# Performance work log

Hardware: AMD Instinct MI355X
Metric: run time of the kernel (lower is better)

The kernel has to match this reference:

```python
import jax, jax.numpy as jnp
import numpy as np

B, N, K, H = 2, 2048, 48, 128
SCALE = 30.0
LN_EPS = 1e-5


def _gather_nodes(nodes, idx):
    # nodes: [B,N,H], idx: [B,N,K] -> [B,N,K,H]
    return nodes[jnp.arange(nodes.shape[0])[:, None, None], idx]


def _ln(x, g, b):
    m = jnp.mean(x, axis=-1, keepdims=True)
    v = jnp.mean(jnp.square(x - m), axis=-1, keepdims=True)
    return (x - m) * jax.lax.rsqrt(v + LN_EPS) * g + b


def _gelu(x):
    return jax.nn.gelu(x, approximate=False)  # torch.nn.GELU default (erf)


def setup_inputs() -> dict:
    key = jax.random.key(0)
    ks = jax.random.split(key, 24)
    d = {}
    d["h_V"] = jax.random.normal(ks[0], (B, N, H), jnp.float32)
    d["h_E"] = jax.random.normal(ks[1], (B, N, K, H), jnp.float32)
    d["E_idx"] = jax.random.randint(ks[2], (B, N, K), 0, N)
    d["mask_V"] = (jax.random.uniform(ks[3], (B, N)) > 0.1).astype(jnp.float32)
    d["mask_attend"] = (jax.random.uniform(ks[4], (B, N, K)) > 0.1).astype(jnp.float32)
    s = 0.05
    # message MLP (node update): W1 in = 3H
    d["W1_w"] = s * jax.random.normal(ks[5], (3 * H, H), jnp.float32)
    d["W1_b"] = jnp.zeros((H,), jnp.float32)
    d["W2_w"] = s * jax.random.normal(ks[6], (H, H), jnp.float32)
    d["W2_b"] = jnp.zeros((H,), jnp.float32)
    d["W3_w"] = s * jax.random.normal(ks[7], (H, H), jnp.float32)
    d["W3_b"] = jnp.zeros((H,), jnp.float32)
    # message MLP (edge update)
    d["W11_w"] = s * jax.random.normal(ks[8], (3 * H, H), jnp.float32)
    d["W11_b"] = jnp.zeros((H,), jnp.float32)
    d["W12_w"] = s * jax.random.normal(ks[9], (H, H), jnp.float32)
    d["W12_b"] = jnp.zeros((H,), jnp.float32)
    d["W13_w"] = s * jax.random.normal(ks[10], (H, H), jnp.float32)
    d["W13_b"] = jnp.zeros((H,), jnp.float32)
    # FFN
    d["Win_w"] = s * jax.random.normal(ks[11], (H, 4 * H), jnp.float32)
    d["Win_b"] = jnp.zeros((4 * H,), jnp.float32)
    d["Wout_w"] = s * jax.random.normal(ks[12], (4 * H, H), jnp.float32)
    d["Wout_b"] = jnp.zeros((H,), jnp.float32)
    # layernorms
    for i, nm in enumerate(["ln1", "ln2", "ln3"]):
        d[nm + "_g"] = jnp.ones((H,), jnp.float32)
        d[nm + "_b"] = jnp.zeros((H,), jnp.float32)
    return d


def reference(h_V, h_E, E_idx, mask_V, mask_attend,
              W1_w, W1_b, W2_w, W2_b, W3_w, W3_b,
              W11_w, W11_b, W12_w, W12_b, W13_w, W13_b,
              Win_w, Win_b, Wout_w, Wout_b,
              ln1_g, ln1_b, ln2_g, ln2_b, ln3_g, ln3_b):
    # --- node message pass ---
    h_EV = jnp.concatenate([
        jnp.broadcast_to(h_V[:, :, None, :], h_E.shape),
        h_E,
        _gather_nodes(h_V, E_idx),
    ], axis=-1)  # [B,N,K,3H]
    h_msg = _gelu(h_EV @ W1_w + W1_b)
    h_msg = _gelu(h_msg @ W2_w + W2_b)
    h_msg = h_msg @ W3_w + W3_b
    h_msg = mask_attend[..., None] * h_msg
    dh = jnp.sum(h_msg, axis=-2) / SCALE  # [B,N,H]
    h_Vn = _ln(h_V + dh, ln1_g, ln1_b)
    # --- FFN ---
    dh = _gelu(h_Vn @ Win_w + Win_b) @ Wout_w + Wout_b
    h_Vn = _ln(h_Vn + dh, ln2_g, ln2_b)
    h_Vn = mask_V[..., None] * h_Vn
    # --- edge update ---
    h_EV2 = jnp.concatenate([
        jnp.broadcast_to(h_Vn[:, :, None, :], h_E.shape),
        h_E,
        _gather_nodes(h_Vn, E_idx),
    ], axis=-1)
    h_msg2 = _gelu(h_EV2 @ W11_w + W11_b)
    h_msg2 = _gelu(h_msg2 @ W12_w + W12_b)
    h_msg2 = h_msg2 @ W13_w + W13_b
    h_En = _ln(h_E + h_msg2, ln3_g, ln3_b)
    return (h_Vn, h_En)
```

## Files before the change

kernel.cpp:

```cpp
#include <hip/hip_runtime.h>
#include <hip/hip_bf16.h>

#define DEVINL __device__ __forceinline__

typedef __attribute__((ext_vector_type(8))) short short8;
typedef __attribute__((ext_vector_type(4))) float f32x4;

DEVINL unsigned short f2bf(float x) {
  __hip_bfloat16 h = __float2bfloat16(x);
  return __builtin_bit_cast(unsigned short, h);
}
DEVINL unsigned int pk2(float lo, float hi) {
  return (unsigned int)f2bf(lo) | ((unsigned int)f2bf(hi) << 16);
}
DEVINL float bf2f(unsigned short h) {
  union { unsigned int u; float f; } c; c.u = ((unsigned int)h) << 16;
  return c.f;
}
DEVINL float gelu_f(float x) {
  const float u = x * x;
  const float y = x * (0.7978845608f + 0.0356774081f * u);
  const float e = __expf(-2.0f * y);
  return x * __builtin_amdgcn_rcpf(1.0f + e);
}
DEVINL f32x4 mfma16(short8 a, short8 b, f32x4 c) {
  return __builtin_amdgcn_mfma_f32_16x16x32_bf16(a, b, c, 0, 0, 0);
}

template<int KSTEPS, int MT, int NT>
DEVINL void gemm_tiles(const unsigned short* Xl, int ldx,
                       const unsigned short* __restrict__ Wp,
                       int lane, int w, f32x4 (&acc)[MT][2])
{
  const int rr = lane & 15;
  const int kg = (lane >> 4) << 3;
  #pragma unroll 2
  for (int t = 0; t < KSTEPS; ++t) {
    short8 a[MT];
    #pragma unroll
    for (int m = 0; m < MT; ++m)
      a[m] = *(const short8*)(Xl + (m * 16 + rr) * ldx + t * 32 + kg);
    #pragma unroll
    for (int c = 0; c < 2; ++c) {
      short8 bf = *(const short8*)(Wp + ((size_t)(t * NT + (w * 2 + c)) * 64 + lane) * 8);
      #pragma unroll
      for (int m = 0; m < MT; ++m)
        acc[m][c] = mfma16(a[m], bf, acc[m][c]);
    }
  }
}

__global__ __launch_bounds__(256) void k_packall(
    const float* __restrict__ W1w,  const float* __restrict__ W2w,
    const float* __restrict__ W3w,  const float* __restrict__ W11w,
    const float* __restrict__ W12w, const float* __restrict__ W13w,
    const float* __restrict__ Winw, const float* __restrict__ Woutw,
    unsigned short* __restrict__ dst)
{
  const int f = blockIdx.x * 256 + threadIdx.x;
  if (f >= 36864) return;
  const float* src; int row0 = 0, Ncols = 128, NT = 8, lf;
  if (f < 20480) {
    const int seg = f >> 11; lf = f & 2047;
    switch (seg) {
      case 0: src = W1w;  row0 = 0;   break;
      case 1: src = W1w;  row0 = 128; break;
      case 2: src = W1w;  row0 = 256; break;
      case 3: src = W2w;  break;
      case 4: src = W3w;  break;
      case 5: src = W11w; row0 = 0;   break;
      case 6: src = W11w; row0 = 128; break;
      case 7: src = W11w; row0 = 256; break;
      case 8: src = W12w; break;
      default: src = W13w; break;
    }
  } else if (f < 28672) { src = Winw; lf = f - 20480; NT = 32; Ncols = 512; }
  else { src = Woutw; lf = f - 28672; }
  const int l = lf & 63;
  const int g = lf >> 6;
  const int c = g % NT;
  const int t = g / NT;
  const int r0 = row0 + t * 32 + ((l >> 4) << 3);
  const int col = c * 16 + (l & 15);
  short8 vv;
  #pragma unroll
  for (int b = 0; b < 8; ++b)
    vv[b] = (short)f2bf(src[(size_t)(r0 + b) * Ncols + col]);
  *(short8*)(dst + (size_t)f * 8) = vv;
}

__global__ __launch_bounds__(256) void k_pre(
    const float* __restrict__ X,
    const unsigned short* __restrict__ Wtp,
    const unsigned short* __restrict__ Wbp,
    const float* __restrict__ bias,
    float* __restrict__ P1, unsigned short* __restrict__ P3)
{
  __shared__ __align__(16) unsigned short Xs2[16 * 136];
  const int tid = threadIdx.x;
  const int lane = tid & 63;
  const int w = tid >> 6;
  const int rr = lane & 15;
  const int kg = (lane >> 4) << 3;
  const int row0 = blockIdx.x * 16;

  for (int e = tid; e < 512; e += 256) {
    const int r = e >> 5, q = (e & 31) << 2;
    float4 v = *(const float4*)(X + (size_t)(row0 + r) * 128 + q);
    uint2 pk; pk.x = pk2(v.x, v.y); pk.y = pk2(v.z, v.w);
    *(uint2*)(&Xs2[r * 136 + q]) = pk;
  }
  __syncthreads();

  const f32x4 zf = {0.f, 0.f, 0.f, 0.f};
  f32x4 a0[2] = {zf, zf}, a1[2] = {zf, zf};
  #pragma unroll
  for (int t = 0; t < 4; ++t) {
    const short8 a = *(const short8*)(&Xs2[rr * 136 + t * 32 + kg]);
    #pragma unroll
    for (int c = 0; c < 2; ++c) {
      short8 bt = *(const short8*)(Wtp + ((size_t)(t * 8 + (w * 2 + c)) * 64 + lane) * 8);
      a0[c] = mfma16(a, bt, a0[c]);
      short8 bb = *(const short8*)(Wbp + ((size_t)(t * 8 + (w * 2 + c)) * 64 + lane) * 8);
      a1[c] = mfma16(a, bb, a1[c]);
    }
  }
  #pragma unroll
  for (int c = 0; c < 2; ++c) {
    const int col = w * 32 + c * 16 + rr;
    const float b = bias[col];
    #pragma unroll
    for (int r = 0; r < 4; ++r) {
      const int row = row0 + ((lane >> 4) << 2) + r;
      P1[(size_t)row * 128 + col] = a0[c][r] + b;
      P3[(size_t)row * 128 + col] = f2bf(a1[c][r]);
    }
  }
}

__global__ __launch_bounds__(256) void k_node(
    const float* __restrict__ hV, const float* __restrict__ hE,
    const int* __restrict__ Eidx, const float* __restrict__ maskA,
    const float* __restrict__ P1g, const unsigned short* __restrict__ P3g,
    const unsigned short* __restrict__ Wmidp,
    const unsigned short* __restrict__ W2p, const float* __restrict__ W2b,
    const unsigned short* __restrict__ W3p, const float* __restrict__ W3b,
    const float* __restrict__ ln1g, const float* __restrict__ ln1b,
    float* __restrict__ hVn1)
{
  __shared__ __align__(16) unsigned short Xs[48 * 136];
  __shared__ __align__(16) unsigned short Ms[48 * 136];
  __shared__ float maskv[48];
  __shared__ float dhs[128];
  __shared__ float red[2];

  const int tid = threadIdx.x;
  const int lane = tid & 63;
  const int w = tid >> 6;
  const int rr = lane & 15;
  const int g4 = (lane >> 4) << 2;
  const int bidx = blockIdx.x;
  const int bbase = bidx & ~2047;

  const float* hErow = hE + (size_t)bidx * 6144;
  const int* idxr = Eidx + (size_t)bidx * 48;

  if (tid < 48) maskv[tid] = maskA[(size_t)bidx * 48 + tid];

  for (int e = tid; e < 1536; e += 256) {
    const int r = e >> 5, q = (e & 31) << 2;
    float4 v = *(const float4*)(hErow + r * 128 + q);
    uint2 pk; pk.x = pk2(v.x, v.y); pk.y = pk2(v.z, v.w);
    *(uint2*)(&Xs[r * 136 + q]) = pk;
  }
  for (int e = tid; e < 768; e += 256) {
    const int r = e >> 4, q = (e & 15) << 3;
    const int j = idxr[r];
    *(short8*)(&Ms[r * 136 + q]) = *(const short8*)(P3g + (size_t)(bbase + j) * 128 + q);
  }
  __syncthreads();

  const float p1c0 = P1g[(size_t)bidx * 128 + w * 32 + rr];
  const float p1c1 = P1g[(size_t)bidx * 128 + w * 32 + 16 + rr];
  f32x4 acc[3][2];
  #pragma unroll
  for (int m = 0; m < 3; ++m)
    #pragma unroll
    for (int c = 0; c < 2; ++c)
      #pragma unroll
      for (int r = 0; r < 4; ++r) {
        const int row = m * 16 + g4 + r;
        const int col = w * 32 + c * 16 + rr;
        acc[m][c][r] = (c ? p1c1 : p1c0) + bf2f(Ms[row * 136 + col]);
      }
  __syncthreads();

  gemm_tiles<4, 3, 8>(Xs, 136, Wmidp, lane, w, acc);
  #pragma unroll
  for (int m = 0; m < 3; ++m)
    #pragma unroll
    for (int c = 0; c < 2; ++c)
      #pragma unroll
      for (int r = 0; r < 4; ++r) {
        const int row = m * 16 + g4 + r;
        Ms[row * 136 + w * 32 + c * 16 + rr] = f2bf(gelu_f(acc[m][c][r]));
      }
  __syncthreads();

  const f32x4 zf = {0.f, 0.f, 0.f, 0.f};
  #pragma unroll
  for (int m = 0; m < 3; ++m) { acc[m][0] = zf; acc[m][1] = zf; }
  gemm_tiles<4, 3, 8>(Ms, 136, W2p, lane, w, acc);
  {
    const float b0 = W2b[w * 32 + rr], b1 = W2b[w * 32 + 16 + rr];
    #pragma unroll
    for (int m = 0; m < 3; ++m)
      #pragma unroll
      for (int c = 0; c < 2; ++c)
        #pragma unroll
        for (int r = 0; r < 4; ++r) {
          const int row = m * 16 + g4 + r;
          Xs[row * 136 + w * 32 + c * 16 + rr] = f2bf(gelu_f(acc[m][c][r] + (c ? b1 : b0)));
        }
  }
  __syncthreads();

  #pragma unroll
  for (int m = 0; m < 3; ++m) { acc[m][0] = zf; acc[m][1] = zf; }
  gemm_tiles<4, 3, 8>(Xs, 136, W3p, lane, w, acc);

  {
    const float b0 = W3b[w * 32 + rr], b1 = W3b[w * 32 + 16 + rr];
    float p0 = 0.f, p1 = 0.f;
    #pragma unroll
    for (int m = 0; m < 3; ++m)
      #pragma unroll
      for (int r = 0; r < 4; ++r) {
        const float mk = maskv[m * 16 + g4 + r];
        p0 += mk * (acc[m][0][r] + b0);
        p1 += mk * (acc[m][1][r] + b1);
      }
    p0 += __shfl_xor(p0, 16); p0 += __shfl_xor(p0, 32);
    p1 += __shfl_xor(p1, 16); p1 += __shfl_xor(p1, 32);
    if (lane < 16) { dhs[w * 32 + lane] = p0; dhs[w * 32 + 16 + lane] = p1; }
  }
  __syncthreads();

  if (tid < 64) {
    const float x0 = hV[(size_t)bidx * 128 + tid]      + dhs[tid]      * (1.0f / 30.0f);
    const float x1 = hV[(size_t)bidx * 128 + 64 + tid] + dhs[tid + 64] * (1.0f / 30.0f);
    float s = x0 + x1, q2 = x0 * x0 + x1 * x1;
    #pragma unroll
    for (int msk = 1; msk < 64; msk <<= 1) {
      s += __shfl_xor(s, msk);
      q2 += __shfl_xor(q2, msk);
    }
    if (tid == 0) {
      const float mean = s * (1.f / 128.f);
      red[0] = mean;
      red[1] = rsqrtf(q2 * (1.f / 128.f) - mean * mean + 1e-5f);
    }
  }
  __syncthreads();
  if (tid < 128) {
    const float x = hV[(size_t)bidx * 128 + tid] + dhs[tid] * (1.0f / 30.0f);
    hVn1[(size_t)bidx * 128 + tid] = (x - red[0]) * red[1] * ln1g[tid] + ln1b[tid];
  }
}

__global__ __launch_bounds__(256) void k_ffn(
    const float* __restrict__ hVn1,
    const unsigned short* __restrict__ Winp, const float* __restrict__ Winb,
    const unsigned short* __restrict__ Woutp, const float* __restrict__ Woutb,
    const float* __restrict__ ln2g, const float* __restrict__ ln2b,
    const float* __restrict__ maskV,
    float* __restrict__ outV)
{
  __shared__ __align__(16) unsigned short Xs2[16 * 136];
  __shared__ __align__(16) unsigned short Ys[16 * 520];
  __shared__ float Rs[16 * 128];

  const int tid = threadIdx.x;
  const int lane = tid & 63;
  const int w = tid >> 6;
  const int rr = lane & 15;
  const int kg = (lane >> 4) << 3;
  const int row0 = blockIdx.x * 16;

  for (int e = tid; e < 512; e += 256) {
    const int r = e >> 5, q = (e & 31) << 2;
    float4 v = *(const float4*)(hVn1 + (size_t)(row0 + r) * 128 + q);
    uint2 pk; pk.x = pk2(v.x, v.y); pk.y = pk2(v.z, v.w);
    *(uint2*)(&Xs2[r * 136 + q]) = pk;
  }
  __syncthreads();

  const f32x4 zf = {0.f, 0.f, 0.f, 0.f};
  f32x4 acc1[8];
  #pragma unroll
  for (int c = 0; c < 8; ++c) acc1[c] = zf;
  #pragma unroll
  for (int t = 0; t < 4; ++t) {
    const short8 a = *(const short8*)(&Xs2[rr * 136 + t * 32 + kg]);
    #pragma unroll
    for (int c = 0; c < 8; ++c) {
      const short8 bf = *(const short8*)(Winp + ((size_t)(t * 32 + w * 8 + c) * 64 + lane) * 8);
      acc1[c] = mfma16(a, bf, acc1[c]);
    }
  }
  #pragma unroll
  for (int c = 0; c < 8; ++c) {
    const int col = w * 128 + c * 16 + rr;
    const float bias = Winb[col];
    #pragma unroll
    for (int r = 0; r < 4; ++r) {
      const int row = ((lane >> 4) << 2) + r;
      Ys[row * 520 + col] = f2bf(gelu_f(acc1[c][r] + bias));
    }
  }
  __syncthreads();

  f32x4 acc2[2];
  acc2[0] = zf; acc2[1] = zf;
  #pragma unroll 4
  for (int t = 0; t < 16; ++t) {
    const short8 a = *(const short8*)(&Ys[rr * 520 + t * 32 + kg]);
    #pragma unroll
    for (int c = 0; c < 2; ++c) {
      const short8 bf = *(const short8*)(Woutp + ((size_t)(t * 8 + w * 2 + c) * 64 + lane) * 8);
      acc2[c] = mfma16(a, bf, acc2[c]);
    }
  }
  #pragma unroll
  for (int c = 0; c < 2; ++c) {
    const int col = w * 32 + c * 16 + rr;
    const float bias = Woutb[col];
    #pragma unroll
    for (int r = 0; r < 4; ++r) {
      const int row = ((lane >> 4) << 2) + r;
      Rs[row * 128 + col] = acc2[c][r] + bias + hVn1[(size_t)(row0 + row) * 128 + col];
    }
  }
  __syncthreads();

  const float g0 = ln2g[lane], g1 = ln2g[lane + 64];
  const float be0 = ln2b[lane], be1 = ln2b[lane + 64];
  for (int i = 0; i < 4; ++i) {
    const int row = w * 4 + i;
    const int grow = row0 + row;
    const float x0 = Rs[row * 128 + lane], x1 = Rs[row * 128 + 64 + lane];
    float s = x0 + x1, q2 = x0 * x0 + x1 * x1;
    #pragma unroll
    for (int msk = 1; msk < 64; msk <<= 1) {
      s += __shfl_xor(s, msk);
      q2 += __shfl_xor(q2, msk);
    }
    const float mean = s * (1.f / 128.f);
    const float rstd = rsqrtf(q2 * (1.f / 128.f) - mean * mean + 1e-5f);
    const float mv = maskV[grow];
    outV[(size_t)grow * 128 + lane]      = ((x0 - mean) * rstd * g0 + be0) * mv;
    outV[(size_t)grow * 128 + 64 + lane] = ((x1 - mean) * rstd * g1 + be1) * mv;
  }
}

__global__ __launch_bounds__(256) void k_edge(
    const float* __restrict__ hE, const int* __restrict__ Eidx,
    const float* __restrict__ P1g, const unsigned short* __restrict__ P3g,
    const unsigned short* __restrict__ Wmidp,
    const unsigned short* __restrict__ W12p, const float* __restrict__ W12b,
    const unsigned short* __restrict__ W13p, const float* __restrict__ W13b,
    const float* __restrict__ ln3g, const float* __restrict__ ln3b,
    float* __restrict__ outE)
{
  __shared__ __align__(16) unsigned short Xs[48 * 136];
  __shared__ __align__(16) unsigned short Ms[48 * 136];
  __shared__ float sums[48 * 4];
  __shared__ float sqs[48 * 4];
  __shared__ float mr[96];

  const int tid = threadIdx.x;
  const int lane = tid & 63;
  const int w = tid >> 6;
  const int rr = lane & 15;
  const int g4 = (lane >> 4) << 2;
  const int bidx = blockIdx.x;
  const int bbase = bidx & ~2047;

  const float* hErow = hE + (size_t)bidx * 6144;
  const int* idxr = Eidx + (size_t)bidx * 48;

  for (int e = tid; e < 1536; e += 256) {
    const int r = e >> 5, q = (e & 31) << 2;
    float4 v = *(const float4*)(hErow + r * 128 + q);
    uint2 pk; pk.x = pk2(v.x, v.y); pk.y = pk2(v.z, v.w);
    *(uint2*)(&Xs[r * 136 + q]) = pk;
  }
  for (int e = tid; e < 768; e += 256) {
    const int r = e >> 4, q = (e & 15) << 3;
    const int j = idxr[r];
    *(short8*)(&Ms[r * 136 + q]) = *(const short8*)(P3g + (size_t)(bbase + j) * 128 + q);
  }
  __syncthreads();

  const float p1c0 = P1g[(size_t)bidx * 128 + w * 32 + rr];
  const float p1c1 = P1g[(size_t)bidx * 128 + w * 32 + 16 + rr];
  f32x4 acc[3][2];
  float res[3][2][4];
  #pragma unroll
  for (int m = 0; m < 3; ++m)
    #pragma unroll
    for (int c = 0; c < 2; ++c)
      #pragma unroll
      for (int r = 0; r < 4; ++r) {
        const int row = m * 16 + g4 + r;
        const int col = w * 32 + c * 16 + rr;
        acc[m][c][r] = (c ? p1c1 : p1c0) + bf2f(Ms[row * 136 + col]);
        res[m][c][r] = bf2f(Xs[row * 136 + col]);
      }
  __syncthreads();

  gemm_tiles<4, 3, 8>(Xs, 136, Wmidp, lane, w, acc);
  #pragma unroll
  for (int m = 0; m < 3; ++m)
    #pragma unroll
    for (int c = 0; c < 2; ++c)
      #pragma unroll
      for (int r = 0; r < 4; ++r) {
        const int row = m * 16 + g4 + r;
        Ms[row * 136 + w * 32 + c * 16 + rr] = f2bf(gelu_f(acc[m][c][r]));
      }
  __syncthreads();

  const f32x4 zf = {0.f, 0.f, 0.f, 0.f};
  #pragma unroll
  for (int m = 0; m < 3; ++m) { acc[m][0] = zf; acc[m][1] = zf; }
  gemm_tiles<4, 3, 8>(Ms, 136, W12p, lane, w, acc);
  {
    const float b0 = W12b[w * 32 + rr], b1 = W12b[w * 32 + 16 + rr];
    #pragma unroll
    for (int m = 0; m < 3; ++m)
      #pragma unroll
      for (int c = 0; c < 2; ++c)
        #pragma unroll
        for (int r = 0; r < 4; ++r) {
          const int row = m * 16 + g4 + r;
          Xs[row * 136 + w * 32 + c * 16 + rr] = f2bf(gelu_f(acc[m][c][r] + (c ? b1 : b0)));
        }
  }
  __syncthreads();

  #pragma unroll
  for (int m = 0; m < 3; ++m) { acc[m][0] = zf; acc[m][1] = zf; }
  gemm_tiles<4, 3, 8>(Xs, 136, W13p, lane, w, acc);

  {
    const float b0 = W13b[w * 32 + rr], b1 = W13b[w * 32 + 16 + rr];
    #pragma unroll
    for (int m = 0; m < 3; ++m)
      #pragma unroll
      for (int r = 0; r < 4; ++r) {
        const int row = m * 16 + g4 + r;
        acc[m][0][r] += b0 + res[m][0][r];
        acc[m][1][r] += b1 + res[m][1][r];
        float s = acc[m][0][r] + acc[m][1][r];
        float q2 = acc[m][0][r] * acc[m][0][r] + acc[m][1][r] * acc[m][1][r];
        s += __shfl_xor(s, 1); q2 += __shfl_xor(q2, 1);
        s += __shfl_xor(s, 2); q2 += __shfl_xor(q2, 2);
        s += __shfl_xor(s, 4); q2 += __shfl_xor(q2, 4);
        s += __shfl_xor(s, 8); q2 += __shfl_xor(q2, 8);
        if ((lane & 15) == 0) { sums[row * 4 + w] = s; sqs[row * 4 + w] = q2; }
      }
  }
  __syncthreads();
  if (tid < 48) {
    const float s = sums[tid * 4] + sums[tid * 4 + 1] + sums[tid * 4 + 2] + sums[tid * 4 + 3];
    const float q2 = sqs[tid * 4] + sqs[tid * 4 + 1] + sqs[tid * 4 + 2] + sqs[tid * 4 + 3];
    const float mean = s * (1.f / 128.f);
    mr[tid * 2] = mean;
    mr[tid * 2 + 1] = rsqrtf(q2 * (1.f / 128.f) - mean * mean + 1e-5f);
  }
  __syncthreads();
  {
    const float g0 = ln3g[w * 32 + rr], g1 = ln3g[w * 32 + 16 + rr];
    const float be0 = ln3b[w * 32 + rr], be1 = ln3b[w * 32 + 16 + rr];
    #pragma unroll
    for (int m = 0; m < 3; ++m)
      #pragma unroll
      for (int r = 0; r < 4; ++r) {
        const int row = m * 16 + g4 + r;
        const float mean = mr[row * 2], rstd = mr[row * 2 + 1];
        const size_t base = (size_t)bidx * 6144 + (size_t)row * 128 + w * 32 + rr;
        outE[base]      = (acc[m][0][r] - mean) * rstd * g0 + be0;
        outE[base + 16] = (acc[m][1][r] - mean) * rstd * g1 + be1;
      }
  }
}

extern "C" void kernel_launch(void* const* d_in, const int* in_sizes, int n_in,
                              void* d_out, int out_size, void* d_ws, size_t ws_size,
                              hipStream_t stream) {
  const float* hV    = (const float*)d_in[0];
  const float* hE    = (const float*)d_in[1];
  const int*   Eidx  = (const int*)d_in[2];
  const float* maskV = (const float*)d_in[3];
  const float* maskA = (const float*)d_in[4];
  const float* W1w  = (const float*)d_in[5];  const float* W1b  = (const float*)d_in[6];
  const float* W2w  = (const float*)d_in[7];  const float* W2b  = (const float*)d_in[8];
  const float* W3w  = (const float*)d_in[9];  const float* W3b  = (const float*)d_in[10];
  const float* W11w = (const float*)d_in[11]; const float* W11b = (const float*)d_in[12];
  const float* W12w = (const float*)d_in[13]; const float* W12b = (const float*)d_in[14];
  const float* W13w = (const float*)d_in[15]; const float* W13b = (const float*)d_in[16];
  const float* Winw = (const float*)d_in[17]; const float* Winb = (const float*)d_in[18];
  const float* Woutw= (const float*)d_in[19]; const float* Woutb= (const float*)d_in[20];
  const float* ln1g = (const float*)d_in[21]; const float* ln1b = (const float*)d_in[22];
  const float* ln2g = (const float*)d_in[23]; const float* ln2b = (const float*)d_in[24];
  const float* ln3g = (const float*)d_in[25]; const float* ln3b = (const float*)d_in[26];

  float* outV = (float*)d_out;
  float* outE = outV + (size_t)4096 * 128;

  char* ws = (char*)d_ws;
  float* hVn1 = (float*)ws;
  float* P1   = (float*)(ws + (size_t)2 * 1024 * 1024);
  unsigned short* P3 = (unsigned short*)(ws + (size_t)4 * 1024 * 1024);
  unsigned short* Wp = (unsigned short*)(ws + (size_t)5 * 1024 * 1024);

  const unsigned short* W1top_p  = Wp;
  const unsigned short* W1mid_p  = Wp + (size_t)2048 * 8;
  const unsigned short* W1bot_p  = Wp + (size_t)4096 * 8;
  const unsigned short* W2p      = Wp + (size_t)6144 * 8;
  const unsigned short* W3p      = Wp + (size_t)8192 * 8;
  const unsigned short* W11top_p = Wp + (size_t)10240 * 8;
  const unsigned short* W11mid_p = Wp + (size_t)12288 * 8;
  const unsigned short* W11bot_p = Wp + (size_t)14336 * 8;
  const unsigned short* W12p     = Wp + (size_t)16384 * 8;
  const unsigned short* W13p     = Wp + (size_t)18432 * 8;
  const unsigned short* Winp     = Wp + (size_t)20480 * 8;
  const unsigned short* Woutp    = Wp + (size_t)28672 * 8;

  k_packall<<<144, 256, 0, stream>>>(W1w, W2w, W3w, W11w, W12w, W13w, Winw, Woutw, Wp);

  k_pre<<<256, 256, 0, stream>>>(hV, W1top_p, W1bot_p, W1b, P1, P3);
  k_node<<<4096, 256, 0, stream>>>(hV, hE, Eidx, maskA, P1, P3,
                                   W1mid_p, W2p, W2b, W3p, W3b,
                                   ln1g, ln1b, hVn1);
  k_ffn<<<256, 256, 0, stream>>>(hVn1, Winp, Winb, Woutp, Woutb,
                                 ln2g, ln2b, maskV, outV);
  k_pre<<<256, 256, 0, stream>>>(outV, W11top_p, W11bot_p, W11b, P1, P3);
  k_edge<<<4096, 256, 0, stream>>>(hE, Eidx, P1, P3,
                                   W11mid_p, W12p, W12b, W13p, W13b,
                                   ln3g, ln3b, outE);
}
```

Baseline: 150.0 us.

## Pre-convert h_E to bf16 once and feed MFMA directly from global memory

A prep kernel now converts h_E from fp32 to a bf16 copy in workspace once. The node and edge kernels then read MFMA A-fragments for the middle W1 slice directly from that global bf16 copy instead of staging them in LDS, which halves the per-kernel h_E read bytes and frees one LDS buffer so more blocks fit per CU. The change also reorders blocks in a strided pattern, fuses the first GELU epilogue into the P1/P3 add, fully unrolls the k-loop, and reads the edge residual from fp32 h_E in the epilogue. In exchange it adds an extra full fp32 read plus a bf16 write of h_E, and it depends on the workspace being large enough, with a fallback path otherwise.

```diff
diff --git a/kernel.cpp b/kernel.cpp
--- a/kernel.cpp
+++ b/kernel.cpp
@@ -34,7 +34,7 @@
 {
   const int rr = lane & 15;
   const int kg = (lane >> 4) << 3;
-  #pragma unroll 2
+  #pragma unroll
   for (int t = 0; t < KSTEPS; ++t) {
     short8 a[MT];
     #pragma unroll
@@ -50,15 +50,51 @@
   }
 }
 
-__global__ __launch_bounds__(256) void k_packall(
+DEVINL void gemm_g(const unsigned short* __restrict__ Ag,
+                   const unsigned short* __restrict__ Wp,
+                   int lane, int w, f32x4 (&acc)[3][2])
+{
+  const int rr = lane & 15;
+  const int kg = (lane >> 4) << 3;
+  #pragma unroll
+  for (int t = 0; t < 4; ++t) {
+    short8 a[3];
+    #pragma unroll
+    for (int m = 0; m < 3; ++m)
+      a[m] = *(const short8*)(Ag + (m * 16 + rr) * 128 + t * 32 + kg);
+    #pragma unroll
+    for (int c = 0; c < 2; ++c) {
+      short8 bf = *(const short8*)(Wp + ((size_t)(t * 8 + (w * 2 + c)) * 64 + lane) * 8);
+      #pragma unroll
+      for (int m = 0; m < 3; ++m)
+        acc[m][c] = mfma16(a[m], bf, acc[m][c]);
+    }
+  }
+}
+
+__global__ __launch_bounds__(256) void k_prep(
     const float* __restrict__ W1w,  const float* __restrict__ W2w,
     const float* __restrict__ W3w,  const float* __restrict__ W11w,
     const float* __restrict__ W12w, const float* __restrict__ W13w,
     const float* __restrict__ Winw, const float* __restrict__ Woutw,
-    unsigned short* __restrict__ dst)
+    unsigned short* __restrict__ dst,
+    const float* __restrict__ hE, unsigned short* __restrict__ hEb)
 {
-  const int f = blockIdx.x * 256 + threadIdx.x;
-  if (f >= 36864) return;
+  const int tid = threadIdx.x;
+  if (blockIdx.x >= 144) {
+    const int bb = blockIdx.x - 144;
+    const float4* s4 = (const float4*)hE;
+    uint2* d2 = (uint2*)hEb;
+    #pragma unroll 4
+    for (int i = 0; i < 12; ++i) {
+      const int idx = bb * 3072 + i * 256 + tid;
+      float4 v = s4[idx];
+      uint2 pk; pk.x = pk2(v.x, v.y); pk.y = pk2(v.z, v.w);
+      d2[idx] = pk;
+    }
+    return;
+  }
+  const int f = blockIdx.x * 256 + tid;
   const float* src; int row0 = 0, Ncols = 128, NT = 8, lf;
   if (f < 20480) {
     const int seg = f >> 11; lf = f & 2047;
@@ -138,8 +174,10 @@
   }
 }
 
-__global__ __launch_bounds__(256) void k_node(
+template<bool DIRECT>
+__global__ __launch_bounds__(256, 6) void k_node_t(
     const float* __restrict__ hV, const float* __restrict__ hE,
+    const unsigned short* __restrict__ hEb,
     const int* __restrict__ Eidx, const float* __restrict__ maskA,
     const float* __restrict__ P1g, const unsigned short* __restrict__ P3g,
     const unsigned short* __restrict__ Wmidp,
@@ -148,8 +186,8 @@
     const float* __restrict__ ln1g, const float* __restrict__ ln1b,
     float* __restrict__ hVn1)
 {
-  __shared__ __align__(16) unsigned short Xs[48 * 136];
   __shared__ __align__(16) unsigned short Ms[48 * 136];
+  __shared__ __align__(16) unsigned short Xs[DIRECT ? 16 : 48 * 136];
   __shared__ float maskv[48];
   __shared__ float dhs[128];
   __shared__ float red[2];
@@ -159,30 +197,40 @@
   const int w = tid >> 6;
   const int rr = lane & 15;
   const int g4 = (lane >> 4) << 2;
-  const int bidx = blockIdx.x;
+  const int bidx = (blockIdx.x & 7) * 512 + (blockIdx.x >> 3);
   const int bbase = bidx & ~2047;
 
-  const float* hErow = hE + (size_t)bidx * 6144;
   const int* idxr = Eidx + (size_t)bidx * 48;
 
   if (tid < 48) maskv[tid] = maskA[(size_t)bidx * 48 + tid];
 
-  for (int e = tid; e < 1536; e += 256) {
-    const int r = e >> 5, q = (e & 31) << 2;
-    float4 v = *(const float4*)(hErow + r * 128 + q);
-    uint2 pk; pk.x = pk2(v.x, v.y); pk.y = pk2(v.z, v.w);
-    *(uint2*)(&Xs[r * 136 + q]) = pk;
+  if constexpr (!DIRECT) {
+    const float* hErow = hE + (size_t)bidx * 6144;
+    for (int e = tid; e < 1536; e += 256) {
+      const int r = e >> 5, q = (e & 31) << 2;
+      float4 v = *(const float4*)(hErow + r * 128 + q);
+      uint2 pk; pk.x = pk2(v.x, v.y); pk.y = pk2(v.z, v.w);
+      *(uint2*)(&Xs[r * 136 + q]) = pk;
+    }
   }
   for (int e = tid; e < 768; e += 256) {
     const int r = e >> 4, q = (e & 15) << 3;
     const int j = idxr[r];
     *(short8*)(&Ms[r * 136 + q]) = *(const short8*)(P3g + (size_t)(bbase + j) * 128 + q);
   }
-  __syncthreads();
-
   const float p1c0 = P1g[(size_t)bidx * 128 + w * 32 + rr];
   const float p1c1 = P1g[(size_t)bidx * 128 + w * 32 + 16 + rr];
+  __syncthreads();
+
+  const f32x4 zf = {0.f, 0.f, 0.f, 0.f};
   f32x4 acc[3][2];
+  #pragma unroll
+  for (int m = 0; m < 3; ++m) { acc[m][0] = zf; acc[m][1] = zf; }
+  if constexpr (DIRECT)
+    gemm_g(hEb + (size_t)bidx * 6144, Wmidp, lane, w, acc);
+  else
+    gemm_tiles<4, 3, 8>(Xs, 136, Wmidp, lane, w, acc);
+
   #pragma unroll
   for (int m = 0; m < 3; ++m)
     #pragma unroll
@@ -191,26 +239,17 @@
       for (int r = 0; r < 4; ++r) {
         const int row = m * 16 + g4 + r;
         const int col = w * 32 + c * 16 + rr;
-        acc[m][c][r] = (c ? p1c1 : p1c0) + bf2f(Ms[row * 136 + col]);
+        const float v = acc[m][c][r] + (c ? p1c1 : p1c0) + bf2f(Ms[row * 136 + col]);
+        Ms[row * 136 + col] = f2bf(gelu_f(v));
       }
   __syncthreads();
 
-  gemm_tiles<4, 3, 8>(Xs, 136, Wmidp, lane, w, acc);
-  #pragma unroll
-  for (int m = 0; m < 3; ++m)
-    #pragma unroll
-    for (int c = 0; c < 2; ++c)
-      #pragma unroll
-      for (int r = 0; r < 4; ++r) {
-        const int row = m * 16 + g4 + r;
-        Ms[row * 136 + w * 32 + c * 16 + rr] = f2bf(gelu_f(acc[m][c][r]));
-      }
-  __syncthreads();
-
-  const f32x4 zf = {0.f, 0.f, 0.f, 0.f};
   #pragma unroll
   for (int m = 0; m < 3; ++m) { acc[m][0] = zf; acc[m][1] = zf; }
   gemm_tiles<4, 3, 8>(Ms, 136, W2p, lane, w, acc);
+  __syncthreads();
+
+  unsigned short* buf2 = DIRECT ? Ms : Xs;
   {
     const float b0 = W2b[w * 32 + rr], b1 = W2b[w * 32 + 16 + rr];
     #pragma unroll
@@ -220,14 +259,14 @@
         #pragma unroll
         for (int r = 0; r < 4; ++r) {
           const int row = m * 16 + g4 + r;
-          Xs[row * 136 + w * 32 + c * 16 + rr] = f2bf(gelu_f(acc[m][c][r] + (c ? b1 : b0)));
+          buf2[row * 136 + w * 32 + c * 16 + rr] = f2bf(gelu_f(acc[m][c][r] + (c ? b1 : b0)));
         }
   }
   __syncthreads();
 
   #pragma unroll
   for (int m = 0; m < 3; ++m) { acc[m][0] = zf; acc[m][1] = zf; }
-  gemm_tiles<4, 3, 8>(Xs, 136, W3p, lane, w, acc);
+  gemm_tiles<4, 3, 8>(buf2, 136, W3p, lane, w, acc);
 
   {
     const float b0 = W3b[w * 32 + rr], b1 = W3b[w * 32 + 16 + rr];
@@ -363,8 +402,10 @@
   }
 }
 
-__global__ __launch_bounds__(256) void k_edge(
-    const float* __restrict__ hE, const int* __restrict__ Eidx,
+template<bool DIRECT>
+__global__ __launch_bounds__(256, 6) void k_edge_t(
+    const float* __restrict__ hE, const unsigned short* __restrict__ hEb,
+    const int* __restrict__ Eidx,
     const float* __restrict__ P1g, const unsigned short* __restrict__ P3g,
     const unsigned short* __restrict__ Wmidp,
     const unsigned short* __restrict__ W12p, const float* __restrict__ W12b,
@@ -372,8 +413,8 @@
     const float* __restrict__ ln3g, const float* __restrict__ ln3b,
     float* __restrict__ outE)
 {
-  __shared__ __align__(16) unsigned short Xs[48 * 136];
   __shared__ __align__(16) unsigned short Ms[48 * 136];
+  __shared__ __align__(16) unsigned short Xs[DIRECT ? 16 : 48 * 136];
   __shared__ float sums[48 * 4];
   __shared__ float sqs[48 * 4];
   __shared__ float mr[96];
@@ -383,29 +424,38 @@
   const int w = tid >> 6;
   const int rr = lane & 15;
   const int g4 = (lane >> 4) << 2;
-  const int bidx = blockIdx.x;
+  const int bidx = (blockIdx.x & 7) * 512 + (blockIdx.x >> 3);
   const int bbase = bidx & ~2047;
 
-  const float* hErow = hE + (size_t)bidx * 6144;
   const int* idxr = Eidx + (size_t)bidx * 48;
 
-  for (int e = tid; e < 1536; e += 256) {
-    const int r = e >> 5, q = (e & 31) << 2;
-    float4 v = *(const float4*)(hErow + r * 128 + q);
-    uint2 pk; pk.x = pk2(v.x, v.y); pk.y = pk2(v.z, v.w);
-    *(uint2*)(&Xs[r * 136 + q]) = pk;
+  if constexpr (!DIRECT) {
+    const float* hErow = hE + (size_t)bidx * 6144;
+    for (int e = tid; e < 1536; e += 256) {
+      const int r = e >> 5, q = (e & 31) << 2;
+      float4 v = *(const float4*)(hErow + r * 128 + q);
+      uint2 pk; pk.x = pk2(v.x, v.y); pk.y = pk2(v.z, v.w);
+      *(uint2*)(&Xs[r * 136 + q]) = pk;
+    }
   }
   for (int e = tid; e < 768; e += 256) {
     const int r = e >> 4, q = (e & 15) << 3;
     const int j = idxr[r];
     *(short8*)(&Ms[r * 136 + q]) = *(const short8*)(P3g + (size_t)(bbase + j) * 128 + q);
   }
-  __syncthreads();
-
   const float p1c0 = P1g[(size_t)bidx * 128 + w * 32 + rr];
   const float p1c1 = P1g[(size_t)bidx * 128 + w * 32 + 16 + rr];
+  __syncthreads();
+
+  const f32x4 zf = {0.f, 0.f, 0.f, 0.f};
   f32x4 acc[3][2];
-  float res[3][2][4];
+  #pragma unroll
+  for (int m = 0; m < 3; ++m) { acc[m][0] = zf; acc[m][1] = zf; }
+  if constexpr (DIRECT)
+    gemm_g(hEb + (size_t)bidx * 6144, Wmidp, lane, w, acc);
+  else
+    gemm_tiles<4, 3, 8>(Xs, 136, Wmidp, lane, w, acc);
+
   #pragma unroll
   for (int m = 0; m < 3; ++m)
     #pragma unroll
@@ -414,27 +464,17 @@
       for (int r = 0; r < 4; ++r) {
         const int row = m * 16 + g4 + r;
         const int col = w * 32 + c * 16 + rr;
-        acc[m][c][r] = (c ? p1c1 : p1c0) + bf2f(Ms[row * 136 + col]);
-        res[m][c][r] = bf2f(Xs[row * 136 + col]);
+        const float v = acc[m][c][r] + (c ? p1c1 : p1c0) + bf2f(Ms[row * 136 + col]);
+        Ms[row * 136 + col] = f2bf(gelu_f(v));
       }
   __syncthreads();
 
-  gemm_tiles<4, 3, 8>(Xs, 136, Wmidp, lane, w, acc);
-  #pragma unroll
-  for (int m = 0; m < 3; ++m)
-    #pragma unroll
-    for (int c = 0; c < 2; ++c)
-      #pragma unroll
-      for (int r = 0; r < 4; ++r) {
-        const int row = m * 16 + g4 + r;
-        Ms[row * 136 + w * 32 + c * 16 + rr] = f2bf(gelu_f(acc[m][c][r]));
-      }
-  __syncthreads();
-
-  const f32x4 zf = {0.f, 0.f, 0.f, 0.f};
   #pragma unroll
   for (int m = 0; m < 3; ++m) { acc[m][0] = zf; acc[m][1] = zf; }
   gemm_tiles<4, 3, 8>(Ms, 136, W12p, lane, w, acc);
+  __syncthreads();
+
+  unsigned short* buf2 = DIRECT ? Ms : Xs;
   {
     const float b0 = W12b[w * 32 + rr], b1 = W12b[w * 32 + 16 + rr];
     #pragma unroll
@@ -444,14 +484,14 @@
         #pragma unroll
         for (int r = 0; r < 4; ++r) {
           const int row = m * 16 + g4 + r;
-          Xs[row * 136 + w * 32 + c * 16 + rr] = f2bf(gelu_f(acc[m][c][r] + (c ? b1 : b0)));
+          buf2[row * 136 + w * 32 + c * 16 + rr] = f2bf(gelu_f(acc[m][c][r] + (c ? b1 : b0)));
         }
   }
   __syncthreads();
 
   #pragma unroll
   for (int m = 0; m < 3; ++m) { acc[m][0] = zf; acc[m][1] = zf; }
-  gemm_tiles<4, 3, 8>(Xs, 136, W13p, lane, w, acc);
+  gemm_tiles<4, 3, 8>(buf2, 136, W13p, lane, w, acc);
 
   {
     const float b0 = W13b[w * 32 + rr], b1 = W13b[w * 32 + 16 + rr];
@@ -460,8 +500,8 @@
       #pragma unroll
       for (int r = 0; r < 4; ++r) {
         const int row = m * 16 + g4 + r;
-        acc[m][0][r] += b0 + res[m][0][r];
-        acc[m][1][r] += b1 + res[m][1][r];
+        acc[m][0][r] += b0 + hE[(size_t)bidx * 6144 + row * 128 + w * 32 + rr];
+        acc[m][1][r] += b1 + hE[(size_t)bidx * 6144 + row * 128 + w * 32 + 16 + rr];
         float s = acc[m][0][r] + acc[m][1][r];
         float q2 = acc[m][0][r] * acc[m][0][r] + acc[m][1][r] * acc[m][1][r];
         s += __shfl_xor(s, 1); q2 += __shfl_xor(q2, 1);
@@ -524,6 +564,10 @@
   float* P1   = (float*)(ws + (size_t)2 * 1024 * 1024);
   unsigned short* P3 = (unsigned short*)(ws + (size_t)4 * 1024 * 1024);
   unsigned short* Wp = (unsigned short*)(ws + (size_t)5 * 1024 * 1024);
+  unsigned short* hEb = (unsigned short*)(ws + (size_t)6 * 1024 * 1024);
+
+  const size_t NEED = (size_t)6 * 1024 * 1024 + (size_t)4096 * 48 * 128 * 2;
+  const bool direct = ws_size >= NEED;
 
   const unsigned short* W1top_p  = Wp;
   const unsigned short* W1mid_p  = Wp + (size_t)2048 * 8;
@@ -538,16 +582,27 @@
   const unsigned short* Winp     = Wp + (size_t)20480 * 8;
   const unsigned short* Woutp    = Wp + (size_t)28672 * 8;
 
-  k_packall<<<144, 256, 0, stream>>>(W1w, W2w, W3w, W11w, W12w, W13w, Winw, Woutw, Wp);
+  k_prep<<<direct ? 2192 : 144, 256, 0, stream>>>(
+      W1w, W2w, W3w, W11w, W12w, W13w, Winw, Woutw, Wp, hE, hEb);
 
   k_pre<<<256, 256, 0, stream>>>(hV, W1top_p, W1bot_p, W1b, P1, P3);
-  k_node<<<4096, 256, 0, stream>>>(hV, hE, Eidx, maskA, P1, P3,
-                                   W1mid_p, W2p, W2b, W3p, W3b,
-                                   ln1g, ln1b, hVn1);
+  if (direct)
+    k_node_t<true><<<4096, 256, 0, stream>>>(hV, hE, hEb, Eidx, maskA, P1, P3,
+                                             W1mid_p, W2p, W2b, W3p, W3b,
+                                             ln1g, ln1b, hVn1);
+  else
+    k_node_t<false><<<4096, 256, 0, stream>>>(hV, hE, hEb, Eidx, maskA, P1, P3,
+                                              W1mid_p, W2p, W2b, W3p, W3b,
+                                              ln1g, ln1b, hVn1);
   k_ffn<<<256, 256, 0, stream>>>(hVn1, Winp, Winb, Woutp, Woutb,
                                  ln2g, ln2b, maskV, outV);
   k_pre<<<256, 256, 0, stream>>>(outV, W11top_p, W11bot_p, W11b, P1, P3);
-  k_edge<<<4096, 256, 0, stream>>>(hE, Eidx, P1, P3,
-                                   W11mid_p, W12p, W12b, W13p, W13b,
-                                   ln3g, ln3b, outE);
-}
+  if (direct)
+    k_edge_t<true><<<4096, 256, 0, stream>>>(hE, hEb, Eidx, P1, P3,
+                                             W11mid_p, W12p, W12b, W13p, W13b,
+                                             ln3g, ln3b, outE);
+  else
+    k_edge_t<false><<<4096, 256, 0, stream>>>(hE, hEb, Eidx, P1, P3,
+                                              W11mid_p, W12p, W12b, W13p, W13b,
+                                              ln3g, ln3b, outE);
+}
```

Measured after the change: 168.8 us. 12.5% more time.
